# Kernel optimization log

Hardware: AMD Instinct MI355X
Metric: run time of the kernel (lower is better)

## Reference

```python
import jax, jax.numpy as jnp
import numpy as np

PADDING = 4


def _grid_sample_bilinear_zeros(img, grid):
    """torch.nn.functional.grid_sample(img, grid, mode='bilinear',
    padding_mode='zeros', align_corners=False).
    img: [N,C,H,W], grid: [N,Ho,Wo,2] with grid[...,0]=x, grid[...,1]=y in [-1,1].
    """
    N, C, H, W = img.shape
    # unnormalize (align_corners=False)
    ix = ((grid[..., 0] + 1.0) * W - 1.0) * 0.5  # [N,Ho,Wo]
    iy = ((grid[..., 1] + 1.0) * H - 1.0) * 0.5
    x0 = jnp.floor(ix)
    y0 = jnp.floor(iy)
    x1 = x0 + 1.0
    y1 = y0 + 1.0
    wx1 = ix - x0
    wx0 = 1.0 - wx1
    wy1 = iy - y0
    wy0 = 1.0 - wy1

    def tap(yy, xx, w):
        valid = (xx >= 0) & (xx < W) & (yy >= 0) & (yy < H)
        xc = jnp.clip(xx, 0, W - 1).astype(jnp.int32)
        yc = jnp.clip(yy, 0, H - 1).astype(jnp.int32)
        # gather per-sample: v[n,c,i,j] = img[n,c,yc[n,i,j],xc[n,i,j]]
        v = jax.vmap(lambda im, y_, x_: im[:, y_, x_])(img, yc, xc)
        return v * (w * valid)[:, None, :, :]

    return (tap(y0, x0, wy0 * wx0) + tap(y0, x1, wy0 * wx1)
            + tap(y1, x0, wy1 * wx0) + tap(y1, x1, wy1 * wx1))


def setup_inputs() -> dict:
    key = jax.random.key(0)
    k1, k2 = jax.random.split(key)
    N, C, H, W = 512, 9, 84, 84
    x = jax.random.normal(k1, (N, C, H, W), dtype=jnp.float32)
    shift = jax.random.randint(k2, (N, 2), 0, 2 * PADDING + 1, dtype=jnp.int32)
    return {"x": x, "shift": shift}


def reference(x, shift):
    n, c, h, w = x.shape
    p = PADDING
    xp = jnp.pad(x, ((0, 0), (0, 0), (p, p), (p, p)))  # zeros pad
    hp = h + 2 * p
    eps = 1.0 / hp
    arange = jnp.linspace(-1.0 + eps, 1.0 - eps, h, dtype=x.dtype)
    # stack(meshgrid(arange, arange, indexing='ij'), -1): [...,0]=row coord,
    # [...,1]=col coord — fed as-is to grid_sample (matches torch code).
    base = jnp.stack(jnp.meshgrid(arange, arange, indexing='ij'), axis=-1)  # [h,h,2]
    sh = shift.astype(x.dtype) * (2.0 / hp)  # [n,2]
    grid = base[None] + sh[:, None, None, :]  # [n,h,h,2]
    return _grid_sample_bilinear_zeros(xp, grid)
```

## Files before the change

kernel.cpp:

```cpp
#include <hip/hip_runtime.h>


constexpr int HW     = 84;
constexpr int LDSW   = 85;
constexpr int NPLANE = HW * HW;

typedef float vfloat4 __attribute__((ext_vector_type(4)));

__device__ __forceinline__ int iclamp(int v, int lo, int hi) {
    return v < lo ? lo : (v > hi ? hi : v);
}

__global__ __launch_bounds__(512) void rshift_kernel(
    const float* __restrict__ x,
    const int*   __restrict__ shift,
    float*       __restrict__ out)
{
    __shared__ float lds[HW * LDSW];

    const int plane = blockIdx.x;
    const int n     = plane / 9;
    const float s0  = (float)shift[2 * n];
    const float s1  = (float)shift[2 * n + 1];
    const float* __restrict__ src = x   + (size_t)plane * NPLANE;
    float*       __restrict__ dst = out + (size_t)plane * NPLANE;
    const int t = threadIdx.x;
    const float R = 91.0f / 83.0f;

    const int lane = t & 63;
    const int wv   = t >> 6;
    const int jq   = lane % 21;
    const int isub = lane / 21;

    float wy0s[4], wy1s[4];
    int   rbase[4];
    #pragma unroll
    for (int e = 0; e < 4; ++e) {
        float fy = fmaf((float)(4 * jq + e), R, s1);
        int   y0 = (int)fy;
        float w1 = fy - (float)y0;
        float w0 = 1.0f - w1;
        int   t0 = y0 - 4;
        int   cb = iclamp(t0, 0, HW - 2);
        wy0s[e] = (t0 == cb) ? w0 : ((t0 + 1 == cb) ? w1 : 0.0f);
        wy1s[e] = (t0 == cb) ? w1 : ((t0 - 1 == cb) ? w0 : 0.0f);
        rbase[e] = cb;
    }

    #pragma unroll
    for (int k = 0; k < 14; ++k) {
        int idx = t + k * 512;
        if (idx < NPLANE) {
            int row = idx / HW;
            int col = idx - row * HW;
            lds[col * LDSW + row] = src[idx];
        }
    }
    __syncthreads();

    if (isub < 3) {
        #pragma unroll
        for (int k = 0; k < 4; ++k) {
            int i = k * 24 + wv * 3 + isub;
            if (i < HW) {
                float fx = fmaf((float)i, R, s0);
                int   x0 = (int)fx;
                float w1 = fx - (float)x0;
                float w0 = 1.0f - w1;
                int   u0 = x0 - 4;
                int   cb = iclamp(u0, 0, HW - 2);
                float wx0 = (u0 == cb) ? w0 : ((u0 + 1 == cb) ? w1 : 0.0f);
                float wx1 = (u0 == cb) ? w1 : ((u0 - 1 == cb) ? w0 : 0.0f);
                int   cu0 = cb * LDSW;
                int   cu1 = cu0 + LDSW;

                vfloat4 o;
                #pragma unroll
                for (int e = 0; e < 4; ++e) {
                    int   b0  = cu0 + rbase[e];
                    int   b1  = cu1 + rbase[e];
                    float v00 = lds[b0];
                    float v01 = lds[b0 + 1];
                    float v10 = lds[b1];
                    float v11 = lds[b1 + 1];
                    o[e] = wx0 * fmaf(wy0s[e], v00, wy1s[e] * v01)
                         + wx1 * fmaf(wy0s[e], v10, wy1s[e] * v11);
                }
                __builtin_nontemporal_store(
                    o, reinterpret_cast<vfloat4*>(dst + (size_t)i * HW + 4 * jq));
            }
        }
    }
}

extern "C" void kernel_launch(void* const* d_in, const int* in_sizes, int n_in,
                              void* d_out, int out_size, void* d_ws, size_t ws_size,
                              hipStream_t stream) {
    const float* x     = (const float*)d_in[0];
    const int*   shift = (const int*)d_in[1];
    float*       out   = (float*)d_out;
    const int planes = 512 * 9;
    rshift_kernel<<<planes, 512, 0, stream>>>(x, shift, out);
}
```

Measured before the change: 45.21 us.

## Compute 4x4 output tiles per thread with column reuse and vectorized loads

```diff
diff --git a/kernel.cpp b/kernel.cpp
--- a/kernel.cpp
+++ b/kernel.cpp
@@ -4,6 +4,7 @@
 constexpr int HW     = 84;
 constexpr int LDSW   = 85;
 constexpr int NPLANE = HW * HW;
+constexpr int NQUADS = NPLANE / 4;
 
 typedef float vfloat4 __attribute__((ext_vector_type(4)));
 
@@ -11,7 +12,7 @@
     return v < lo ? lo : (v > hi ? hi : v);
 }
 
-__global__ __launch_bounds__(512) void rshift_kernel(
+__global__ __launch_bounds__(448) void rshift_kernel(
     const float* __restrict__ x,
     const int*   __restrict__ shift,
     float*       __restrict__ out)
@@ -27,13 +28,29 @@
     const int t = threadIdx.x;
     const float R = 91.0f / 83.0f;
 
+    #pragma unroll
+    for (int k = 0; k < 4; ++k) {
+        int q = t + k * 448;
+        if (q < NQUADS) {
+            int row  = q / 21;
+            int col0 = (q - row * 21) * 4;
+            vfloat4 v = *reinterpret_cast<const vfloat4*>(src + q * 4);
+            int b = col0 * LDSW + row;
+            lds[b]            = v.x;
+            lds[b + LDSW]     = v.y;
+            lds[b + 2 * LDSW] = v.z;
+            lds[b + 3 * LDSW] = v.w;
+        }
+    }
+
     const int lane = t & 63;
     const int wv   = t >> 6;
     const int jq   = lane % 21;
-    const int isub = lane / 21;
+    const int iq   = wv * 3 + lane / 21;
+    const bool active = (lane != 63);
 
     float wy0s[4], wy1s[4];
-    int   rbase[4];
+    int   rr[4];
     #pragma unroll
     for (int e = 0; e < 4; ++e) {
         float fy = fmaf((float)(4 * jq + e), R, s1);
@@ -44,51 +61,63 @@
         int   cb = iclamp(t0, 0, HW - 2);
         wy0s[e] = (t0 == cb) ? w0 : ((t0 + 1 == cb) ? w1 : 0.0f);
         wy1s[e] = (t0 == cb) ? w1 : ((t0 - 1 == cb) ? w0 : 0.0f);
-        rbase[e] = cb;
+        rr[e] = cb;
     }
 
+    float wx0s[4], wx1s[4];
+    int   pa[4];
+    int   cbase = 0;
     #pragma unroll
-    for (int k = 0; k < 14; ++k) {
-        int idx = t + k * 512;
-        if (idx < NPLANE) {
-            int row = idx / HW;
-            int col = idx - row * HW;
-            lds[col * LDSW + row] = src[idx];
-        }
+    for (int a = 0; a < 4; ++a) {
+        float fx = fmaf((float)(4 * iq + a), R, s0);
+        int   x0 = (int)fx;
+        float w1 = fx - (float)x0;
+        float w0 = 1.0f - w1;
+        int   u0 = x0 - 4;
+        int   cb = iclamp(u0, 0, HW - 2);
+        if (a == 0) cbase = iclamp(u0, 0, HW - 6);
+        wx0s[a] = (u0 == cb) ? w0 : ((u0 + 1 == cb) ? w1 : 0.0f);
+        wx1s[a] = (u0 == cb) ? w1 : ((u0 - 1 == cb) ? w0 : 0.0f);
+        pa[a]   = cb - cbase;
     }
+
     __syncthreads();
 
-    if (isub < 3) {
+    if (active) {
+        float acc[4][4];
         #pragma unroll
-        for (int k = 0; k < 4; ++k) {
-            int i = k * 24 + wv * 3 + isub;
-            if (i < HW) {
-                float fx = fmaf((float)i, R, s0);
-                int   x0 = (int)fx;
-                float w1 = fx - (float)x0;
-                float w0 = 1.0f - w1;
-                int   u0 = x0 - 4;
-                int   cb = iclamp(u0, 0, HW - 2);
-                float wx0 = (u0 == cb) ? w0 : ((u0 + 1 == cb) ? w1 : 0.0f);
-                float wx1 = (u0 == cb) ? w1 : ((u0 - 1 == cb) ? w0 : 0.0f);
-                int   cu0 = cb * LDSW;
-                int   cu1 = cu0 + LDSW;
+        for (int a = 0; a < 4; ++a)
+            #pragma unroll
+            for (int e = 0; e < 4; ++e) acc[a][e] = 0.0f;
 
-                vfloat4 o;
+        const int base = cbase * LDSW;
+        #pragma unroll
+        for (int c = 0; c < 6; ++c) {
+            const int caddr = base + c * LDSW;
+            float yc[4];
+            #pragma unroll
+            for (int e = 0; e < 4; ++e) {
+                float v0 = lds[caddr + rr[e]];
+                float v1 = lds[caddr + rr[e] + 1];
+                yc[e] = wy0s[e] * v0 + wy1s[e] * v1;
+            }
+            #pragma unroll
+            for (int a = 0; a < 4; ++a) {
+                float w = (c == pa[a]) ? wx0s[a]
+                        : ((c == pa[a] + 1) ? wx1s[a] : 0.0f);
                 #pragma unroll
-                for (int e = 0; e < 4; ++e) {
-                    int   b0  = cu0 + rbase[e];
-                    int   b1  = cu1 + rbase[e];
-                    float v00 = lds[b0];
-                    float v01 = lds[b0 + 1];
-                    float v10 = lds[b1];
-                    float v11 = lds[b1 + 1];
-                    o[e] = wx0 * fmaf(wy0s[e], v00, wy1s[e] * v01)
-                         + wx1 * fmaf(wy0s[e], v10, wy1s[e] * v11);
-                }
-                __builtin_nontemporal_store(
-                    o, reinterpret_cast<vfloat4*>(dst + (size_t)i * HW + 4 * jq));
+                for (int e = 0; e < 4; ++e)
+                    acc[a][e] = fmaf(w, yc[e], acc[a][e]);
             }
+        }
+
+        #pragma unroll
+        for (int a = 0; a < 4; ++a) {
+            vfloat4 o;
+            o.x = acc[a][0]; o.y = acc[a][1]; o.z = acc[a][2]; o.w = acc[a][3];
+            __builtin_nontemporal_store(
+                o, reinterpret_cast<vfloat4*>(
+                       dst + (size_t)(4 * iq + a) * HW + 4 * jq));
         }
     }
 }
@@ -100,5 +129,5 @@
     const int*   shift = (const int*)d_in[1];
     float*       out   = (float*)d_out;
     const int planes = 512 * 9;
-    rshift_kernel<<<planes, 512, 0, stream>>>(x, shift, out);
+    rshift_kernel<<<planes, 448, 0, stream>>>(x, shift, out);
 }
```

After: 47.22 us. +4.5%, slower.

## Process three planes per block with double-buffered LDS and vectorized loads

Applied to the files above, without the earlier changes.

```diff
diff --git a/kernel.cpp b/kernel.cpp
--- a/kernel.cpp
+++ b/kernel.cpp
@@ -4,6 +4,7 @@
 constexpr int HW     = 84;
 constexpr int LDSW   = 85;
 constexpr int NPLANE = HW * HW;
+constexpr int NQUADS = NPLANE / 4;
 
 typedef float vfloat4 __attribute__((ext_vector_type(4)));
 
@@ -16,16 +17,19 @@
     const int*   __restrict__ shift,
     float*       __restrict__ out)
 {
-    __shared__ float lds[HW * LDSW];
+    __shared__ float lds[2][HW * LDSW];
 
-    const int plane = blockIdx.x;
-    const int n     = plane / 9;
-    const float s0  = (float)shift[2 * n];
-    const float s1  = (float)shift[2 * n + 1];
-    const float* __restrict__ src = x   + (size_t)plane * NPLANE;
-    float*       __restrict__ dst = out + (size_t)plane * NPLANE;
-    const int t = threadIdx.x;
-    const float R = 91.0f / 83.0f;
+    const int blk = blockIdx.x;
+    const int n   = blk / 3;
+    const int c0  = (blk - n * 3) * 3;
+    const float s0 = (float)shift[2 * n];
+    const float s1 = (float)shift[2 * n + 1];
+    const float R  = 91.0f / 83.0f;
+    const int t    = threadIdx.x;
+
+    const size_t pbase = ((size_t)n * 9 + c0) * NPLANE;
+    const float* __restrict__ src = x   + pbase;
+    float*       __restrict__ dst = out + pbase;
 
     const int lane = t & 63;
     const int wv   = t >> 6;
@@ -33,7 +37,7 @@
     const int isub = lane / 21;
 
     float wy0s[4], wy1s[4];
-    int   rbase[4];
+    int   rr[4];
     #pragma unroll
     for (int e = 0; e < 4; ++e) {
         float fy = fmaf((float)(4 * jq + e), R, s1);
@@ -44,51 +48,83 @@
         int   cb = iclamp(t0, 0, HW - 2);
         wy0s[e] = (t0 == cb) ? w0 : ((t0 + 1 == cb) ? w1 : 0.0f);
         wy1s[e] = (t0 == cb) ? w1 : ((t0 - 1 == cb) ? w0 : 0.0f);
-        rbase[e] = cb;
+        rr[e] = cb;
     }
 
+    float wx0h[4], wx1h[4];
+    int   cu0h[4];
+    bool  iok[4];
     #pragma unroll
-    for (int k = 0; k < 14; ++k) {
-        int idx = t + k * 512;
-        if (idx < NPLANE) {
-            int row = idx / HW;
-            int col = idx - row * HW;
-            lds[col * LDSW + row] = src[idx];
-        }
+    for (int k = 0; k < 4; ++k) {
+        int i  = k * 24 + wv * 3 + isub;
+        iok[k] = (isub < 3) && (i < HW);
+        float fx = fmaf((float)i, R, s0);
+        int   x0 = (int)fx;
+        float w1 = fx - (float)x0;
+        float w0 = 1.0f - w1;
+        int   u0 = x0 - 4;
+        int   cb = iclamp(u0, 0, HW - 2);
+        wx0h[k] = (u0 == cb) ? w0 : ((u0 + 1 == cb) ? w1 : 0.0f);
+        wx1h[k] = (u0 == cb) ? w1 : ((u0 - 1 == cb) ? w0 : 0.0f);
+        cu0h[k] = cb * LDSW;
     }
-    __syncthreads();
 
-    if (isub < 3) {
+    auto loadp = [&](int p, vfloat4& a0, vfloat4& a1, vfloat4& a2, vfloat4& a3) {
+        const float* s = src + (size_t)p * NPLANE;
+        a0 = *reinterpret_cast<const vfloat4*>(s + 4 * t);
+        a1 = *reinterpret_cast<const vfloat4*>(s + 4 * (t + 512));
+        a2 = *reinterpret_cast<const vfloat4*>(s + 4 * (t + 1024));
+        if (t < NQUADS - 1536)
+            a3 = *reinterpret_cast<const vfloat4*>(s + 4 * (t + 1536));
+    };
+    auto put1 = [&](float* buf, int q, vfloat4 v) {
+        int row  = q / 21;
+        int col0 = (q - row * 21) * 4;
+        int b    = col0 * LDSW + row;
+        buf[b]            = v.x;
+        buf[b + LDSW]     = v.y;
+        buf[b + 2 * LDSW] = v.z;
+        buf[b + 3 * LDSW] = v.w;
+    };
+    auto writep = [&](float* buf, vfloat4 a0, vfloat4 a1, vfloat4 a2, vfloat4 a3) {
+        put1(buf, t,        a0);
+        put1(buf, t + 512,  a1);
+        put1(buf, t + 1024, a2);
+        if (t < NQUADS - 1536) put1(buf, t + 1536, a3);
+    };
+    auto computep = [&](int p, const float* buf) {
+        float* d = dst + (size_t)p * NPLANE;
         #pragma unroll
         for (int k = 0; k < 4; ++k) {
-            int i = k * 24 + wv * 3 + isub;
-            if (i < HW) {
-                float fx = fmaf((float)i, R, s0);
-                int   x0 = (int)fx;
-                float w1 = fx - (float)x0;
-                float w0 = 1.0f - w1;
-                int   u0 = x0 - 4;
-                int   cb = iclamp(u0, 0, HW - 2);
-                float wx0 = (u0 == cb) ? w0 : ((u0 + 1 == cb) ? w1 : 0.0f);
-                float wx1 = (u0 == cb) ? w1 : ((u0 - 1 == cb) ? w0 : 0.0f);
-                int   cu0 = cb * LDSW;
-                int   cu1 = cu0 + LDSW;
-
+            if (iok[k]) {
+                int i = k * 24 + wv * 3 + isub;
                 vfloat4 o;
                 #pragma unroll
                 for (int e = 0; e < 4; ++e) {
-                    int   b0  = cu0 + rbase[e];
-                    int   b1  = cu1 + rbase[e];
-                    float v00 = lds[b0];
-                    float v01 = lds[b0 + 1];
-                    float v10 = lds[b1];
-                    float v11 = lds[b1 + 1];
-                    o[e] = wx0 * fmaf(wy0s[e], v00, wy1s[e] * v01)
-                         + wx1 * fmaf(wy0s[e], v10, wy1s[e] * v11);
+                    int   b0 = cu0h[k] + rr[e];
+                    int   b1 = b0 + LDSW;
+                    o[e] = wx0h[k] * fmaf(wy0s[e], buf[b0], wy1s[e] * buf[b0 + 1])
+                         + wx1h[k] * fmaf(wy0s[e], buf[b1], wy1s[e] * buf[b1 + 1]);
                 }
                 __builtin_nontemporal_store(
-                    o, reinterpret_cast<vfloat4*>(dst + (size_t)i * HW + 4 * jq));
+                    o, reinterpret_cast<vfloat4*>(d + (size_t)i * HW + 4 * jq));
             }
+        }
+    };
+
+    vfloat4 a0, a1, a2, a3;
+    loadp(0, a0, a1, a2, a3);
+    writep(&lds[0][0], a0, a1, a2, a3);
+    __syncthreads();
+
+    #pragma unroll
+    for (int p = 0; p < 3; ++p) {
+        vfloat4 b0, b1, b2, b3;
+        if (p < 2) loadp(p + 1, b0, b1, b2, b3);
+        computep(p, &lds[p & 1][0]);
+        if (p < 2) {
+            writep(&lds[(p + 1) & 1][0], b0, b1, b2, b3);
+            __syncthreads();
         }
     }
 }
@@ -99,6 +135,6 @@
     const float* x     = (const float*)d_in[0];
     const int*   shift = (const int*)d_in[1];
     float*       out   = (float*)d_out;
-    const int planes = 512 * 9;
-    rshift_kernel<<<planes, 512, 0, stream>>>(x, shift, out);
+    const int blocks = 512 * 3;
+    rshift_kernel<<<blocks, 512, 0, stream>>>(x, shift, out);
 }
```

Result: no change. 44.48 us (-1.6%).
